# Performance work log

Measured on AMD Instinct MI355X. Metric: run time of the kernel, lower is better.

## Reference

```python
import jax, jax.numpy as jnp
import numpy as np

B, S, DIN = 2, 2048, 1024
H = 16
DK = 1024   # dim_key_query_all
DV = 1024   # dim_value_all
DOUT = 1024
HEAD_SIZE = DK / H  # attention_head_size (float division in source)
LN_EPS = 1e-5


def setup_inputs() -> dict:
    key = jax.random.key(0)
    ks = jax.random.split(key, 12)
    s_in = 1.0 / np.sqrt(DIN)
    s_dv = 1.0 / np.sqrt(DV)
    return {
        "hidden_states": jax.random.normal(ks[0], (B, S, DIN), jnp.float32),
        "Wq": jax.random.uniform(ks[1], (DK, DIN), jnp.float32, -s_in, s_in),
        "Wk": jax.random.uniform(ks[2], (DK, DIN), jnp.float32, -s_in, s_in),
        "Wcb": jax.random.uniform(ks[3], (H, DIN), jnp.float32, -s_in, s_in),
        "Wv": jax.random.uniform(ks[4], (DV, DIN), jnp.float32, -s_in, s_in),
        "bv": jax.random.uniform(ks[5], (DV,), jnp.float32, -s_in, s_in),
        "mixing": 0.2 * jax.random.normal(ks[6], (H, DK), jnp.float32),
        "Wd": jax.random.uniform(ks[7], (DOUT, DV), jnp.float32, -s_dv, s_dv),
        "bd": jax.random.uniform(ks[8], (DOUT,), jnp.float32, -s_dv, s_dv),
        "gamma": jnp.ones((DV,), jnp.float32),
        "beta": jnp.zeros((DV,), jnp.float32),
    }


def reference(hidden_states, Wq, Wk, Wcb, Wv, bv, mixing, Wd, bd, gamma, beta):
    x = hidden_states  # [B, S, DIN]; self-attention: from == to
    q = jnp.einsum('bsd,kd->bsk', x, Wq)  # [B,S,DK]
    k = jnp.einsum('bsd,kd->bsk', x, Wk)  # [B,S,DK]
    # scores[b,h,i,j] = sum_c q[b,i,c]*mixing[h,c]*k[b,j,c]
    scores = jnp.einsum('bic,hc,bjc->bhij', q, mixing, k)
    cb = jnp.einsum('bjd,hd->bhj', x, Wcb)  # content bias [B,H,S]
    scores = scores + cb[:, :, None, :]
    scores = scores / jnp.sqrt(jnp.asarray(HEAD_SIZE, scores.dtype))
    probs = jax.nn.softmax(scores, axis=-1)  # dropout p=0.0 -> identity
    v = jnp.einsum('bsd,vd->bsv', x, Wv) + bv  # [B,S,DV]
    v = v.reshape(B, S, H, DV // H)
    ctx = jnp.einsum('bhij,bjhv->bihv', probs, v).reshape(B, S, DV)
    out = jnp.einsum('bsv,ov->bso', ctx, Wd) + bd
    res = x + out
    mu = jnp.mean(res, axis=-1, keepdims=True)
    var = jnp.var(res, axis=-1, keepdims=True)
    out = (res - mu) * jax.lax.rsqrt(var + LN_EPS) * gamma + beta
    return (out,)
```

## Files before the change

### kernel.cpp

```cpp
#include <hip/hip_runtime.h>
#include <cstddef>
#include <cstdint>

#define B_    2
#define S_    2048
#define DIN_  1024
#define H_    16
#define DK_   1024
#define DV_   1024
#define DH_   64
#define DOUT_ 1024
#define M_    (B_ * S_)

typedef __attribute__((ext_vector_type(8)))  short short8;
typedef __attribute__((ext_vector_type(4)))  float float4v;
typedef __attribute__((ext_vector_type(16))) float float16v;
typedef _Float16 half8v __attribute__((ext_vector_type(8)));

__device__ __forceinline__ float bf16s_to_f(short s) {
  union { unsigned int u; float f; } cv;
  cv.u = ((unsigned int)(unsigned short)s) << 16;
  return cv.f;
}
__device__ __forceinline__ short f_to_bf16s(float f) {
  union { float f; unsigned int u; } cv;
  cv.f = f;
  unsigned int u = cv.u + 0x7FFFu + ((cv.u >> 16) & 1u);
  return (short)(u >> 16);
}
__device__ __forceinline__ short f_to_f16s(float f) {
  union { _Float16 h; short s; } cv;
  cv.h = (_Float16)f;
  return cv.s;
}
__device__ __forceinline__ unsigned pkrtz_u32(float a, float b) {
  union { __fp16 __attribute__((ext_vector_type(2))) h2; unsigned u; } cv;
  cv.h2 = __builtin_amdgcn_cvt_pkrtz(a, b);
  return cv.u;
}
__device__ __forceinline__ void gll16(const void* g, void* l) {
  __builtin_amdgcn_global_load_lds(
      (const __attribute__((address_space(1))) unsigned int*)g,
      (__attribute__((address_space(3))) unsigned int*)l, 16, 0, 0);
}

__global__ __launch_bounds__(256) void cast_kernel(const float* __restrict__ in,
                                                   short* __restrict__ out, int n4) {
  int i = blockIdx.x * 256 + threadIdx.x;
  if (i >= n4) return;
  float4 v = ((const float4*)in)[i];
  union { ushort4 u; short s[4]; } o;
  o.s[0] = f_to_bf16s(v.x); o.s[1] = f_to_bf16s(v.y);
  o.s[2] = f_to_bf16s(v.z); o.s[3] = f_to_bf16s(v.w);
  ((ushort4*)out)[i] = o.u;
}

__global__ __launch_bounds__(256) void cb_kernel(const float* __restrict__ x,
                                                 const float* __restrict__ Wcb,
                                                 float* __restrict__ CBs) {
  __shared__ float xs[DIN_];
  const int row = blockIdx.x;
  const int tid = threadIdx.x;
  #pragma unroll
  for (int it = 0; it < 4; ++it)
    xs[tid + it * 256] = x[(size_t)row * DIN_ + tid + it * 256];
  __syncthreads();
  const int lane = tid & 63, w = tid >> 6;
  const float SC = 0.125f * 1.44269504088896f;
  #pragma unroll
  for (int hh = 0; hh < 4; ++hh) {
    const int hidx = w * 4 + hh;
    float p = 0.f;
    for (int c = lane; c < DIN_; c += 64)
      p += xs[c] * Wcb[(size_t)hidx * DIN_ + c];
    #pragma unroll
    for (int mk = 1; mk < 64; mk <<= 1) p += __shfl_xor(p, mk);
    if (lane == 0) {
      const int bb = row / S_, ss = row % S_;
      CBs[((size_t)bb * H_ + hidx) * S_ + ss] = p * SC;
    }
  }
}

__global__ __launch_bounds__(256, 4) void gemm_nt(
    const short* __restrict__ A, const short* __restrict__ Bw,
    const float* __restrict__ bias, const float* __restrict__ resid,
    short* __restrict__ outb, float* __restrict__ outf, int mode) {
  const int KD = 1024, ND = 1024;
  __shared__ __align__(16) short As[64 * 128];
  __shared__ __align__(16) short Bs[64 * 128];
  const int tid  = threadIdx.x;
  const int lane = tid & 63;
  const int w    = tid >> 6;
  const int quad = lane >> 4;
  const int l16  = lane & 15;
  const int m0   = blockIdx.y * 64;
  const int n0   = blockIdx.x * 64;
  const int wm   = (w >> 1) * 32;
  const int wn   = (w & 1) * 32;

  const int drow = lane >> 4;
  const int dp   = lane & 15;

  const float4v zero = {0.f, 0.f, 0.f, 0.f};
  float4v acc[2][2];
  acc[0][0] = zero; acc[0][1] = zero; acc[1][0] = zero; acc[1][1] = zero;

  for (int k0 = 0; k0 < KD; k0 += 128) {
    __syncthreads();
    #pragma unroll
    for (int cc = 0; cc < 4; ++cc) {
      const int n = w * 4 + cc;
      const int r = 4 * n + drow;
      const int l = dp ^ (r & 15);
      gll16(A  + (size_t)(m0 + r) * KD + k0 + l * 8, &As[n * 512]);
      gll16(Bw + (size_t)(n0 + r) * KD + k0 + l * 8, &Bs[n * 512]);
    }
    __syncthreads();
    #pragma unroll
    for (int ks = 0; ks < 4; ++ks) {
      const int ca = ((ks * 4 + quad) ^ l16) * 8;
      short8 af0 = *(short8*)&As[(wm + l16) * 128 + ca];
      short8 af1 = *(short8*)&As[(wm + 16 + l16) * 128 + ca];
      short8 bg0 = *(short8*)&Bs[(wn + l16) * 128 + ca];
      short8 bg1 = *(short8*)&Bs[(wn + 16 + l16) * 128 + ca];
      acc[0][0] = __builtin_amdgcn_mfma_f32_16x16x32_bf16(af0, bg0, acc[0][0], 0, 0, 0);
      acc[0][1] = __builtin_amdgcn_mfma_f32_16x16x32_bf16(af0, bg1, acc[0][1], 0, 0, 0);
      acc[1][0] = __builtin_amdgcn_mfma_f32_16x16x32_bf16(af1, bg0, acc[1][0], 0, 0, 0);
      acc[1][1] = __builtin_amdgcn_mfma_f32_16x16x32_bf16(af1, bg1, acc[1][1], 0, 0, 0);
    }
  }

  #pragma unroll
  for (int mt = 0; mt < 2; ++mt)
    #pragma unroll
    for (int nt = 0; nt < 2; ++nt)
      #pragma unroll
      for (int r = 0; r < 4; ++r) {
        int row = m0 + wm + mt * 16 + quad * 4 + r;
        int col = n0 + wn + nt * 16 + l16;
        float v = acc[mt][nt][r];
        if (mode == 1 || mode == 5) v += bias[col];
        if (mode == 2)
          outf[(size_t)row * ND + col] = v + bias[col] + resid[(size_t)row * ND + col];
        else if (mode == 5) {
          int bb = row >> 11, ss = row & 2047;
          outb[((size_t)bb * DV_ + col) * S_ + ss] = f_to_f16s(v);
        } else if (mode == 6) {
          short* dst = outb + ((col >> 10) ? (size_t)M_ * 1024 : 0) +
                       (size_t)row * 1024 + (col & 1023);
          *dst = f_to_f16s(v);
        } else if (mode == 4)
          outb[(size_t)row * ND + col] = f_to_f16s(v);
        else
          outb[(size_t)row * ND + col] = f_to_bf16s(v);
      }
}

__global__ __launch_bounds__(256, 2) void attn_kernel(
    const short* __restrict__ Qf, const short* __restrict__ Kf,
    const short* __restrict__ Vtf, const float* __restrict__ mixing,
    const float* __restrict__ CBs, short* __restrict__ ctxb) {
  __shared__ __align__(16) short KsF[2 * 128 * 64];
  __shared__ __align__(16) short Vt[64][136];
  __shared__ __align__(16) short mix_s[DK_];
  __shared__ float cb_s[128];

  const int tid  = threadIdx.x;
  const int lane = tid & 63;
  const int l32  = lane & 31;
  const int l1   = lane >> 5;
  const int w    = tid >> 6;

  const int F    = blockIdx.x;
  const int xcd  = F & 7, rest = F >> 3;
  const int b    = xcd >> 2;
  const int h    = (xcd & 3) * 4 + (rest & 3);
  const int i0   = (rest >> 2) * 128;

  const float SC = 0.125f * 1.44269504088896f;
  for (int c = tid; c < DK_; c += 256) {
    union { _Float16 h; short s; } cv;
    cv.h = (_Float16)(mixing[(size_t)h * DK_ + c] * SC);
    mix_s[c] = cv.s;
  }

  const int iq = i0 + w * 32 + l32;
  const short* qptr  = Qf + ((size_t)b * S_ + iq) * DK_;
  const short* kbase = Kf + (size_t)b * S_ * DK_;
  const short* vtb   = Vtf + ((size_t)b * DV_ + h * DH_) * S_;
  const float* cbp   = CBs + ((size_t)b * H_ + h) * S_;

  float16v accS[4], accO[2];
  #pragma unroll
  for (int g = 0; g < 2; ++g)
    #pragma unroll
    for (int r = 0; r < 16; ++r) accO[g][r] = 0.f;
  float m_run = -1e30f, l_run = 0.f;

  const int nrow = lane >> 3;
  const int dp8  = lane & 7;

  const int vrow = tid >> 2;
  const int vseg = (tid & 3) * 32;

  for (int j0 = 0; j0 < S_; j0 += 128) {
    short8 vreg[4];
    #pragma unroll
    for (int c = 0; c < 4; ++c)
      vreg[c] = *(const short8*)(vtb + (size_t)vrow * S_ + j0 + vseg + c * 8);
    float cbv = 0.f;
    if (tid < 128) cbv = cbp[j0 + tid];
    __syncthreads();
    #pragma unroll
    for (int c = 0; c < 4; ++c)
      *(short8*)&Vt[vrow][vseg + c * 8] = vreg[c];
    if (tid < 128) cb_s[tid] = cbv;

    #pragma unroll
    for (int cc = 0; cc < 4; ++cc) {
      const int n = w * 4 + cc;
      const int r = 8 * n + nrow;
      const int lchunk = dp8 ^ (r & 7);
      gll16(kbase + (size_t)(j0 + r) * DK_ + lchunk * 8, &KsF[n * 512]);
    }
    half8v qcur[4], qnext[4];
    #pragma unroll
    for (int ks = 0; ks < 4; ++ks) {
      qcur[ks] = *(const half8v*)(qptr + ks * 16 + l1 * 8);
      qnext[ks] = qcur[ks];
    }

    #pragma unroll
    for (int f = 0; f < 4; ++f)
      #pragma unroll
      for (int r = 0; r < 16; ++r) accS[f][r] = 0.f;

    __syncthreads();

    for (int t = 0; t < 16; ++t) {
      if (t < 15) {
        const int nb = (t + 1) & 1;
        #pragma unroll
        for (int cc = 0; cc < 4; ++cc) {
          const int n = w * 4 + cc;
          const int r = 8 * n + nrow;
          const int lchunk = dp8 ^ (r & 7);
          gll16(kbase + (size_t)(j0 + r) * DK_ + (t + 1) * 64 + lchunk * 8,
                &KsF[nb * 8192 + n * 512]);
        }
        #pragma unroll
        for (int ks = 0; ks < 4; ++ks)
          qnext[ks] = *(const half8v*)(qptr + (t + 1) * 64 + ks * 16 + l1 * 8);
      }
      const short* kb = &KsF[(t & 1) * 8192];
      __builtin_amdgcn_s_setprio(1);
      #pragma unroll
      for (int ks = 0; ks < 4; ++ks) {
        half8v mf = *(half8v*)&mix_s[t * 64 + ks * 16 + l1 * 8];
        half8v qm = qcur[ks] * mf;
        const int poff = (((2 * ks + l1) ^ (l32 & 7)) * 8) + l32 * 64;
        #pragma unroll
        for (int f = 0; f < 4; ++f) {
          half8v af = *(half8v*)&kb[f * 2048 + poff];
          accS[f] = __builtin_amdgcn_mfma_f32_32x32x16_f16(af, qm, accS[f], 0, 0, 0);
        }
      }
      __builtin_amdgcn_s_setprio(0);
      #pragma unroll
      for (int ks = 0; ks < 4; ++ks) qcur[ks] = qnext[ks];
      __syncthreads();
    }

    float tmax = -1e30f;
    #pragma unroll
    for (int f = 0; f < 4; ++f)
      #pragma unroll
      for (int q = 0; q < 4; ++q) {
        float4 cbq = *(float4*)&cb_s[f * 32 + q * 8 + l1 * 4];
        #pragma unroll
        for (int c = 0; c < 4; ++c) {
          accS[f][4 * q + c] += ((const float*)&cbq)[c];
          tmax = fmaxf(tmax, accS[f][4 * q + c]);
        }
      }
    tmax = fmaxf(tmax, __shfl_xor(tmax, 32));
    const float mnew = fmaxf(m_run, tmax);
    const float alpha = exp2f(m_run - mnew);
    float tsum = 0.f;
    #pragma unroll
    for (int f = 0; f < 4; ++f)
      #pragma unroll
      for (int r = 0; r < 16; ++r) {
        float pv = exp2f(accS[f][r] - mnew);
        accS[f][r] = pv;
        tsum += pv;
      }
    tsum += __shfl_xor(tsum, 32);
    l_run = l_run * alpha + tsum;
    m_run = mnew;
    #pragma unroll
    for (int g = 0; g < 2; ++g)
      #pragma unroll
      for (int r = 0; r < 16; ++r) accO[g][r] *= alpha;

    #pragma unroll
    for (int cpv = 0; cpv < 8; ++cpv) {
      const int t = cpv & 1, fp = cpv >> 1;
      float xo[4], yo[4], lo[4], hi[4];
      #pragma unroll
      for (int c = 0; c < 4; ++c) {
        xo[c] = __shfl_xor(accS[fp][8 * t + c], 32);
        yo[c] = __shfl_xor(accS[fp][8 * t + 4 + c], 32);
      }
      #pragma unroll
      for (int c = 0; c < 4; ++c) {
        lo[c] = l1 ? yo[c] : accS[fp][8 * t + c];
        hi[c] = l1 ? accS[fp][8 * t + 4 + c] : xo[c];
      }
      union { half8v v; unsigned u[4]; } pb;
      pb.u[0] = pkrtz_u32(lo[0], lo[1]);
      pb.u[1] = pkrtz_u32(lo[2], lo[3]);
      pb.u[2] = pkrtz_u32(hi[0], hi[1]);
      pb.u[3] = pkrtz_u32(hi[2], hi[3]);
      #pragma unroll
      for (int g = 0; g < 2; ++g) {
        half8v vf = *(half8v*)&Vt[g * 32 + l32][cpv * 16 + l1 * 8];
        accO[g] = __builtin_amdgcn_mfma_f32_32x32x16_f16(vf, pb.v, accO[g], 0, 0, 0);
      }
    }
  }

  const float rl = 1.0f / l_run;
  short* cbase = ctxb + ((size_t)b * S_ + iq) * DV_ + h * DH_;
  #pragma unroll
  for (int g = 0; g < 2; ++g)
    #pragma unroll
    for (int q = 0; q < 4; ++q) {
      const int dv = g * 32 + 8 * q + 4 * l1;
      union { ushort4 u4; short s[4]; } ov;
      #pragma unroll
      for (int r = 0; r < 4; ++r)
        ov.s[r] = f_to_bf16s(accO[g][4 * q + r] * rl);
      *(ushort4*)(cbase + dv) = ov.u4;
    }
}

__global__ __launch_bounds__(256) void ln_kernel(float* __restrict__ out,
                                                 const float* __restrict__ gamma,
                                                 const float* __restrict__ beta) {
  __shared__ float red[8];
  const int row = blockIdx.x;
  const int tid = threadIdx.x;
  float* p = out + (size_t)row * DOUT_;
  float4 v = ((const float4*)p)[tid];
  float s = v.x + v.y + v.z + v.w;
  #pragma unroll
  for (int mk = 1; mk < 64; mk <<= 1) s += __shfl_xor(s, mk);
  if ((tid & 63) == 0) red[tid >> 6] = s;
  __syncthreads();
  const float mean = (red[0] + red[1] + red[2] + red[3]) * (1.0f / 1024.0f);
  const float d0 = v.x - mean, d1 = v.y - mean, d2 = v.z - mean, d3 = v.w - mean;
  float sq = d0 * d0 + d1 * d1 + d2 * d2 + d3 * d3;
  #pragma unroll
  for (int mk = 1; mk < 64; mk <<= 1) sq += __shfl_xor(sq, mk);
  if ((tid & 63) == 0) red[4 + (tid >> 6)] = sq;
  __syncthreads();
  const float var = (red[4] + red[5] + red[6] + red[7]) * (1.0f / 1024.0f);
  const float rstd = rsqrtf(var + 1e-5f);
  float4 g = ((const float4*)gamma)[tid];
  float4 bt = ((const float4*)beta)[tid];
  float4 o;
  o.x = d0 * rstd * g.x + bt.x;
  o.y = d1 * rstd * g.y + bt.y;
  o.z = d2 * rstd * g.z + bt.z;
  o.w = d3 * rstd * g.w + bt.w;
  ((float4*)p)[tid] = o;
}

extern "C" void kernel_launch(void* const* d_in, const int* in_sizes, int n_in,
                              void* d_out, int out_size, void* d_ws, size_t ws_size,
                              hipStream_t stream) {
  (void)in_sizes; (void)n_in; (void)out_size; (void)ws_size;
  const float* x      = (const float*)d_in[0];
  const float* Wq     = (const float*)d_in[1];
  const float* Wk     = (const float*)d_in[2];
  const float* Wcb    = (const float*)d_in[3];
  const float* Wv     = (const float*)d_in[4];
  const float* bv     = (const float*)d_in[5];
  const float* mixing = (const float*)d_in[6];
  const float* Wd     = (const float*)d_in[7];
  const float* bd     = (const float*)d_in[8];
  const float* gamma  = (const float*)d_in[9];
  const float* beta   = (const float*)d_in[10];
  float* out = (float*)d_out;

  short* p = (short*)d_ws;
  short* xb   = p; p += (size_t)M_ * DIN_;
  short* Qf   = p; p += (size_t)M_ * DK_;
  short* Kf   = p; p += (size_t)M_ * DK_;
  short* Vtf  = p; p += (size_t)B_ * DV_ * S_;
  short* ctxb = p; p += (size_t)M_ * DV_;
  short* Wqb  = p; p += (size_t)DK_ * DIN_;
  short* Wkb  = p; p += (size_t)DK_ * DIN_;
  short* Wvb  = p; p += (size_t)DV_ * DIN_;
  short* Wdb  = p; p += (size_t)DOUT_ * DV_;
  float* CBs  = (float*)p;
  (void)Kf; (void)Wkb;

  cast_kernel<<<dim3(M_ * DIN_ / 1024), 256, 0, stream>>>(x, xb, M_ * DIN_ / 4);
  cast_kernel<<<dim3(DK_ * DIN_ / 1024), 256, 0, stream>>>(Wq, Wqb, DK_ * DIN_ / 4);
  cast_kernel<<<dim3(DK_ * DIN_ / 1024), 256, 0, stream>>>(Wk, Wkb, DK_ * DIN_ / 4);
  cast_kernel<<<dim3(DV_ * DIN_ / 1024), 256, 0, stream>>>(Wv, Wvb, DV_ * DIN_ / 4);
  cast_kernel<<<dim3(DOUT_ * DV_ / 1024), 256, 0, stream>>>(Wd, Wdb, DOUT_ * DV_ / 4);
  cb_kernel<<<dim3(M_), 256, 0, stream>>>(x, Wcb, CBs);

  dim3 gqk(2048 / 64, M_ / 64);
  gemm_nt<<<gqk, 256, 0, stream>>>(xb, Wqb, nullptr, nullptr, Qf, nullptr, 6);
  dim3 gg(DOUT_ / 64, M_ / 64);
  gemm_nt<<<gg, 256, 0, stream>>>(xb, Wvb, bv, nullptr, Vtf, nullptr, 5);

  attn_kernel<<<dim3(512), 256, 0, stream>>>(Qf, Kf, Vtf, mixing, CBs, ctxb);

  gemm_nt<<<gg, 256, 0, stream>>>(ctxb, Wdb, bd, x, nullptr, out, 2);
  ln_kernel<<<dim3(M_), 256, 0, stream>>>(out, gamma, beta);
}
```

Measured before the change: 623.2 us.

## Triple-buffer K tiles in attention QK loop with vmcnt-gated barriers

The K-tile staging buffer in LDS grows from two to three slots. Global-to-LDS loads are now issued two k-steps ahead instead of one, and the full __syncthreads in the loop is replaced by an explicit s_waitcnt vmcnt plus s_barrier. The aim is to hide more global-load latency behind the MFMA work and avoid draining every outstanding memory op at each step. The cost is an extra 16 KB of LDS per block, which could limit occupancy. Correctness also now depends on the vmcnt counts matching the exact order in which loads are issued.

```diff
diff --git a/kernel.cpp b/kernel.cpp
--- a/kernel.cpp
+++ b/kernel.cpp
@@ -161,7 +161,7 @@
     const short* __restrict__ Qf, const short* __restrict__ Kf,
     const short* __restrict__ Vtf, const float* __restrict__ mixing,
     const float* __restrict__ CBs, short* __restrict__ ctxb) {
-  __shared__ __align__(16) short KsF[2 * 128 * 64];
+  __shared__ __align__(16) short KsF[3 * 128 * 64];
   __shared__ __align__(16) short Vt[64][136];
   __shared__ __align__(16) short mix_s[DK_];
   __shared__ float cb_s[128];
@@ -224,6 +224,14 @@
       const int lchunk = dp8 ^ (r & 7);
       gll16(kbase + (size_t)(j0 + r) * DK_ + lchunk * 8, &KsF[n * 512]);
     }
+    #pragma unroll
+    for (int cc = 0; cc < 4; ++cc) {
+      const int n = w * 4 + cc;
+      const int r = 8 * n + nrow;
+      const int lchunk = dp8 ^ (r & 7);
+      gll16(kbase + (size_t)(j0 + r) * DK_ + 64 + lchunk * 8,
+            &KsF[8192 + n * 512]);
+    }
     half8v qcur[4], qnext[4];
     #pragma unroll
     for (int ks = 0; ks < 4; ++ks) {
@@ -236,24 +244,30 @@
       #pragma unroll
       for (int r = 0; r < 16; ++r) accS[f][r] = 0.f;
 
-    __syncthreads();
-
+    __builtin_amdgcn_sched_barrier(0);
+    asm volatile("s_waitcnt vmcnt(8) lgkmcnt(0)" ::: "memory");
+    __builtin_amdgcn_s_barrier();
+    __builtin_amdgcn_sched_barrier(0);
+
+    int rd = 0;
     for (int t = 0; t < 16; ++t) {
-      if (t < 15) {
-        const int nb = (t + 1) & 1;
+      if (t < 14) {
+        int wr = rd + 2; if (wr >= 3) wr -= 3;
         #pragma unroll
         for (int cc = 0; cc < 4; ++cc) {
           const int n = w * 4 + cc;
           const int r = 8 * n + nrow;
           const int lchunk = dp8 ^ (r & 7);
-          gll16(kbase + (size_t)(j0 + r) * DK_ + (t + 1) * 64 + lchunk * 8,
-                &KsF[nb * 8192 + n * 512]);
+          gll16(kbase + (size_t)(j0 + r) * DK_ + (t + 2) * 64 + lchunk * 8,
+                &KsF[wr * 8192 + n * 512]);
         }
+      }
+      if (t < 15) {
         #pragma unroll
         for (int ks = 0; ks < 4; ++ks)
           qnext[ks] = *(const half8v*)(qptr + (t + 1) * 64 + ks * 16 + l1 * 8);
       }
-      const short* kb = &KsF[(t & 1) * 8192];
+      const short* kb = &KsF[rd * 8192];
       __builtin_amdgcn_s_setprio(1);
       #pragma unroll
       for (int ks = 0; ks < 4; ++ks) {
@@ -269,7 +283,14 @@
       __builtin_amdgcn_s_setprio(0);
       #pragma unroll
       for (int ks = 0; ks < 4; ++ks) qcur[ks] = qnext[ks];
-      __syncthreads();
+      if (t < 15) {
+        __builtin_amdgcn_sched_barrier(0);
+        if (t < 14) asm volatile("s_waitcnt vmcnt(8)" ::: "memory");
+        else        asm volatile("s_waitcnt vmcnt(4)" ::: "memory");
+        __builtin_amdgcn_s_barrier();
+        __builtin_amdgcn_sched_barrier(0);
+      }
+      rd = (rd + 1 == 3) ? 0 : rd + 1;
     }
 
     float tmax = -1e30f;
```

Result: no change. 617.0 us, median of 2 (-1.0%).

## Widen K chunks, pipeline K loads across tiles, read V directly from global

Applied to the files above, without the earlier changes.

The attention kernel now stages K in 128-wide d-chunks with a double buffer that keeps prefetching across key-tile boundaries. Explicit vmcnt waits plus raw s_barrier replace __syncthreads, so the prefetch stays in flight while the current chunk is consumed. The V shared-memory tile is removed and V fragments are loaded straight from global memory for the PV MFMAs. This cuts the per-tile pipeline drain and the LDS staging of V, at the cost of uncoalesced global V reads, more registers for the Q fragments, and hand-tuned waitcnt correctness.

```diff
diff --git a/kernel.cpp b/kernel.cpp
--- a/kernel.cpp
+++ b/kernel.cpp
@@ -161,8 +161,7 @@
     const short* __restrict__ Qf, const short* __restrict__ Kf,
     const short* __restrict__ Vtf, const float* __restrict__ mixing,
     const float* __restrict__ CBs, short* __restrict__ ctxb) {
-  __shared__ __align__(16) short KsF[2 * 128 * 64];
-  __shared__ __align__(16) short Vt[64][136];
+  __shared__ __align__(16) short KsF[2 * 128 * 128];
   __shared__ __align__(16) short mix_s[DK_];
   __shared__ float cb_s[128];
 
@@ -180,8 +179,8 @@
 
   const float SC = 0.125f * 1.44269504088896f;
   for (int c = tid; c < DK_; c += 256) {
-    union { _Float16 h; short s; } cv;
-    cv.h = (_Float16)(mixing[(size_t)h * DK_ + c] * SC);
+    union { _Float16 hh; short s; } cv;
+    cv.hh = (_Float16)(mixing[(size_t)h * DK_ + c] * SC);
     mix_s[c] = cv.s;
   }
 
@@ -198,78 +197,88 @@
     for (int r = 0; r < 16; ++r) accO[g][r] = 0.f;
   float m_run = -1e30f, l_run = 0.f;
 
-  const int nrow = lane >> 3;
-  const int dp8  = lane & 7;
-
-  const int vrow = tid >> 2;
-  const int vseg = (tid & 3) * 32;
-
-  for (int j0 = 0; j0 < S_; j0 += 128) {
-    short8 vreg[4];
-    #pragma unroll
-    for (int c = 0; c < 4; ++c)
-      vreg[c] = *(const short8*)(vtb + (size_t)vrow * S_ + j0 + vseg + c * 8);
+  const int drow = lane >> 4;
+  const int dp   = lane & 15;
+
+  #pragma unroll
+  for (int cc = 0; cc < 8; ++cc) {
+    const int n = w * 8 + cc;
+    const int r = 4 * n + drow;
+    const int l = dp ^ (r & 15);
+    gll16(kbase + (size_t)r * DK_ + l * 8, &KsF[n * 512]);
+  }
+  __builtin_amdgcn_sched_barrier(0);
+  half8v qcur[8], qnext[8];
+  #pragma unroll
+  for (int ks = 0; ks < 8; ++ks) {
+    qcur[ks] = *(const half8v*)(qptr + ks * 16 + l1 * 8);
+    qnext[ks] = qcur[ks];
+  }
+  __builtin_amdgcn_sched_barrier(0);
+  asm volatile("s_waitcnt vmcnt(8) lgkmcnt(0)" ::: "memory");
+  __builtin_amdgcn_s_barrier();
+  __builtin_amdgcn_sched_barrier(0);
+
+  for (int jt = 0; jt < 16; ++jt) {
+    const int j0 = jt * 128;
     float cbv = 0.f;
     if (tid < 128) cbv = cbp[j0 + tid];
-    __syncthreads();
-    #pragma unroll
-    for (int c = 0; c < 4; ++c)
-      *(short8*)&Vt[vrow][vseg + c * 8] = vreg[c];
+    if (jt > 0) {
+      __builtin_amdgcn_sched_barrier(0);
+      asm volatile("s_waitcnt vmcnt(8) lgkmcnt(0)" ::: "memory");
+      __builtin_amdgcn_s_barrier();
+      __builtin_amdgcn_sched_barrier(0);
+    }
     if (tid < 128) cb_s[tid] = cbv;
 
     #pragma unroll
-    for (int cc = 0; cc < 4; ++cc) {
-      const int n = w * 4 + cc;
-      const int r = 8 * n + nrow;
-      const int lchunk = dp8 ^ (r & 7);
-      gll16(kbase + (size_t)(j0 + r) * DK_ + lchunk * 8, &KsF[n * 512]);
-    }
-    half8v qcur[4], qnext[4];
-    #pragma unroll
-    for (int ks = 0; ks < 4; ++ks) {
-      qcur[ks] = *(const half8v*)(qptr + ks * 16 + l1 * 8);
-      qnext[ks] = qcur[ks];
-    }
-
-    #pragma unroll
     for (int f = 0; f < 4; ++f)
       #pragma unroll
       for (int r = 0; r < 16; ++r) accS[f][r] = 0.f;
 
-    __syncthreads();
-
-    for (int t = 0; t < 16; ++t) {
-      if (t < 15) {
-        const int nb = (t + 1) & 1;
+    for (int t = 0; t < 8; ++t) {
+      const int g = jt * 8 + t;
+      if (g < 127) {
+        const int g1 = g + 1;
+        const int j1 = (g1 >> 3) * 128, t1 = g1 & 7;
         #pragma unroll
-        for (int cc = 0; cc < 4; ++cc) {
-          const int n = w * 4 + cc;
-          const int r = 8 * n + nrow;
-          const int lchunk = dp8 ^ (r & 7);
-          gll16(kbase + (size_t)(j0 + r) * DK_ + (t + 1) * 64 + lchunk * 8,
-                &KsF[nb * 8192 + n * 512]);
+        for (int cc = 0; cc < 8; ++cc) {
+          const int n = w * 8 + cc;
+          const int r = 4 * n + drow;
+          const int l = dp ^ (r & 15);
+          gll16(kbase + (size_t)(j1 + r) * DK_ + t1 * 128 + l * 8,
+                &KsF[(g1 & 1) * 16384 + n * 512]);
         }
+      }
+      __builtin_amdgcn_sched_barrier(0);
+      if (g < 127) {
+        const int t1 = (g + 1) & 7;
         #pragma unroll
-        for (int ks = 0; ks < 4; ++ks)
-          qnext[ks] = *(const half8v*)(qptr + (t + 1) * 64 + ks * 16 + l1 * 8);
-      }
-      const short* kb = &KsF[(t & 1) * 8192];
+        for (int ks = 0; ks < 8; ++ks)
+          qnext[ks] = *(const half8v*)(qptr + t1 * 128 + ks * 16 + l1 * 8);
+      }
+      const short* kb = &KsF[(g & 1) * 16384];
       __builtin_amdgcn_s_setprio(1);
       #pragma unroll
-      for (int ks = 0; ks < 4; ++ks) {
-        half8v mf = *(half8v*)&mix_s[t * 64 + ks * 16 + l1 * 8];
+      for (int ks = 0; ks < 8; ++ks) {
+        half8v mf = *(half8v*)&mix_s[t * 128 + ks * 16 + l1 * 8];
         half8v qm = qcur[ks] * mf;
-        const int poff = (((2 * ks + l1) ^ (l32 & 7)) * 8) + l32 * 64;
+        const int poff = (((2 * ks + l1) ^ (l32 & 15)) * 8) + l32 * 128;
         #pragma unroll
         for (int f = 0; f < 4; ++f) {
-          half8v af = *(half8v*)&kb[f * 2048 + poff];
+          half8v af = *(half8v*)&kb[f * 4096 + poff];
           accS[f] = __builtin_amdgcn_mfma_f32_32x32x16_f16(af, qm, accS[f], 0, 0, 0);
         }
       }
       __builtin_amdgcn_s_setprio(0);
       #pragma unroll
-      for (int ks = 0; ks < 4; ++ks) qcur[ks] = qnext[ks];
-      __syncthreads();
+      for (int ks = 0; ks < 8; ++ks) qcur[ks] = qnext[ks];
+      if (t < 7) {
+        __builtin_amdgcn_sched_barrier(0);
+        asm volatile("s_waitcnt vmcnt(8) lgkmcnt(0)" ::: "memory");
+        __builtin_amdgcn_s_barrier();
+        __builtin_amdgcn_sched_barrier(0);
+      }
     }
 
     float tmax = -1e30f;
@@ -306,17 +315,17 @@
 
     #pragma unroll
     for (int cpv = 0; cpv < 8; ++cpv) {
-      const int t = cpv & 1, fp = cpv >> 1;
+      const int tt = cpv & 1, fp = cpv >> 1;
       float xo[4], yo[4], lo[4], hi[4];
       #pragma unroll
       for (int c = 0; c < 4; ++c) {
-        xo[c] = __shfl_xor(accS[fp][8 * t + c], 32);
-        yo[c] = __shfl_xor(accS[fp][8 * t + 4 + c], 32);
+        xo[c] = __shfl_xor(accS[fp][8 * tt + c], 32);
+        yo[c] = __shfl_xor(accS[fp][8 * tt + 4 + c], 32);
       }
       #pragma unroll
       for (int c = 0; c < 4; ++c) {
-        lo[c] = l1 ? yo[c] : accS[fp][8 * t + c];
-        hi[c] = l1 ? accS[fp][8 * t + 4 + c] : xo[c];
+        lo[c] = l1 ? yo[c] : accS[fp][8 * tt + c];
+        hi[c] = l1 ? accS[fp][8 * tt + 4 + c] : xo[c];
       }
       union { half8v v; unsigned u[4]; } pb;
       pb.u[0] = pkrtz_u32(lo[0], lo[1]);
@@ -325,7 +334,8 @@
       pb.u[3] = pkrtz_u32(hi[2], hi[3]);
       #pragma unroll
       for (int g = 0; g < 2; ++g) {
-        half8v vf = *(half8v*)&Vt[g * 32 + l32][cpv * 16 + l1 * 8];
+        half8v vf = *(const half8v*)(vtb + (size_t)(g * 32 + l32) * S_ +
+                                     j0 + cpv * 16 + l1 * 8);
         accO[g] = __builtin_amdgcn_mfma_f32_32x32x16_f16(vf, pb.v, accO[g], 0, 0, 0);
       }
     }
```

Result: slower. 637.6 us (+2.3%).
